# Kernel optimization log

Measured on AMD Instinct MI355X. Metric: run time of the kernel, lower is better.

## Reference

```python
import jax, jax.numpy as jnp
import numpy as np
import math

B, S, D, H, L, V, MAXLEN = 4, 2047, 256, 8, 2, 32000, 2048
DK = D // H
DFF = 2 * D
EPS = 1e-5


def make_pe(max_len, d):
    pos = jnp.arange(max_len, dtype=jnp.float32)[:, None]
    div = jnp.exp(jnp.arange(0, d, 2, dtype=jnp.float32) * (-math.log(10000.0) / d))
    pe = jnp.zeros((max_len, d), dtype=jnp.float32)
    pe = pe.at[:, 0::2].set(jnp.sin(pos * div))
    pe = pe.at[:, 1::2].set(jnp.cos(pos * div))
    return pe[None]  # [1, max_len, d]


def setup_inputs() -> dict:
    key = jax.random.key(0)
    ks = jax.random.split(key, 16)
    s = 0.02
    T = S + 1
    return {
        "embeddings": jax.random.normal(ks[0], (B, D), jnp.float32),
        "output_tokens": jax.random.randint(ks[1], (B, S), 0, V, jnp.int64),
        "causal_mask": jnp.tril(jnp.ones((T, T), jnp.int32))[None, None],  # [1,1,T,T]
        "key_padding_mask": jnp.ones((B, 1, 1, T), jnp.int32),
        "tok_emb": jax.random.normal(ks[2], (V, D), jnp.float32) * s,
        "pe": make_pe(MAXLEN, D),
        "Wq": jax.random.normal(ks[3], (L, D, D), jnp.float32) * s,
        "Wk": jax.random.normal(ks[4], (L, D, D), jnp.float32) * s,
        "Wv": jax.random.normal(ks[5], (L, D, D), jnp.float32) * s,
        "Wo": jax.random.normal(ks[6], (L, D, D), jnp.float32) * s,
        "bo": jnp.zeros((L, D), jnp.float32),
        "ln1_g": jnp.ones((L, D), jnp.float32),
        "ln1_b": jnp.zeros((L, D), jnp.float32),
        "W1": jax.random.normal(ks[7], (L, D, DFF), jnp.float32) * s,
        "b1": jnp.zeros((L, DFF), jnp.float32),
        "W2": jax.random.normal(ks[8], (L, DFF, D), jnp.float32) * s,
        "b2": jnp.zeros((L, D), jnp.float32),
        "ln2_g": jnp.ones((L, D), jnp.float32),
        "ln2_b": jnp.zeros((L, D), jnp.float32),
    }


def layer_norm(x, g, b):
    mu = jnp.mean(x, axis=-1, keepdims=True)
    var = jnp.mean(jnp.square(x - mu), axis=-1, keepdims=True)
    return (x - mu) * jax.lax.rsqrt(var + EPS) * g + b


def attention(x, Wq, Wk, Wv, Wo, bo, causal_mask, key_padding_mask):
    b, t, d = x.shape
    q = (x @ Wq).reshape(b, t, H, DK)
    k = (x @ Wk).reshape(b, t, H, DK)
    v = (x @ Wv).reshape(b, t, H, DK)
    scores = jnp.einsum('bqhd,bkhd->bhqk', q, k) / math.sqrt(DK)  # [B,H,T,T]
    neg = jnp.float32(-jnp.inf)
    scores = jnp.where(causal_mask == 0, neg, scores)
    scores = jnp.where(key_padding_mask == 0, neg, scores)
    attn = jax.nn.softmax(scores, axis=-1)
    out = jnp.einsum('bhqk,bkhd->bqhd', attn, v).reshape(b, t, d)
    return out @ Wo + bo


def reference(embeddings, output_tokens, causal_mask, key_padding_mask,
              tok_emb, pe, Wq, Wk, Wv, Wo, bo, ln1_g, ln1_b,
              W1, b1, W2, b2, ln2_g, ln2_b):
    emb_tok = tok_emb[output_tokens]                       # [B,S,D]
    x = jnp.concatenate([embeddings[:, None, :], emb_tok], axis=1)  # [B,T,D]
    x = x + pe[:, :x.shape[1]]
    for l in range(L):
        a = attention(x, Wq[l], Wk[l], Wv[l], Wo[l], bo[l], causal_mask, key_padding_mask)
        x = layer_norm(x + a, ln1_g[l], ln1_b[l])
        ff = jax.nn.relu(x @ W1[l] + b1[l]) @ W2[l] + b2[l]
        x = layer_norm(x + ff, ln2_g[l], ln2_b[l])
    return x[:, 1:, :]  # drop the prepended embedding position
```

## Files before the change

### kernel.cpp

```cpp
#include <hip/hip_runtime.h>
#include <cstdint>
#include <cstddef>

#define B_   4
#define S_   2047
#define T_   2048
#define D_   256
#define H_   8
#define DK_  32
#define DFF_ 512
#define L_   2

typedef short          s8v  __attribute__((ext_vector_type(8)));
typedef float          f4v  __attribute__((ext_vector_type(4)));
typedef unsigned short u8v  __attribute__((ext_vector_type(8)));
typedef unsigned int   u2v  __attribute__((ext_vector_type(2)));
typedef unsigned int   uint32;

union U8 { u8v v; unsigned short e[8]; };

__device__ __forceinline__ float bf2f(unsigned short h) {
    unsigned int u = ((unsigned int)h) << 16;
    float f; __builtin_memcpy(&f, &u, 4); return f;
}
__device__ __forceinline__ unsigned short f2bf(float f) {
    unsigned int u; __builtin_memcpy(&u, &f, 4);
    u += 0x7fffu + ((u >> 16) & 1u);
    return (unsigned short)(u >> 16);
}
__device__ __forceinline__ uint32 pack_bf2(float lo, float hi) {
    uint32 a, b;
    __builtin_memcpy(&a, &lo, 4); __builtin_memcpy(&b, &hi, 4);
    a += 0x8000u; b += 0x8000u;
    return __builtin_amdgcn_perm(b, a, 0x07060302);
}

#define QSCALE2 0.25503485951542068f

__global__ __launch_bounds__(256) void prep_k(
    const float* __restrict__ emb, const int* __restrict__ toks,
    const float* __restrict__ tokE, const float* __restrict__ pe,
    unsigned short* __restrict__ X,
    const float* __restrict__ Wq, const float* __restrict__ Wk,
    const float* __restrict__ Wv, const float* __restrict__ Wo,
    const float* __restrict__ W1, const float* __restrict__ W2,
    unsigned short* __restrict__ WqkvT, unsigned short* __restrict__ WoT,
    unsigned short* __restrict__ W1T, unsigned short* __restrict__ W2T)
{
    __shared__ float tile[32][33];
    if (blockIdx.x < 1024) {
        int idx = blockIdx.x * 256 + threadIdx.x;
        int d8 = (idx & 31) * 8;
        int t  = (idx >> 5) & (T_ - 1);
        int b  = idx >> 16;
        const float* src = (t == 0) ? (emb + b * D_)
                                    : (tokE + (size_t)toks[b * S_ + t - 1] * D_);
        const float* p = pe + (size_t)t * D_ + d8;
        U8 o;
#pragma unroll
        for (int j = 0; j < 8; ++j) o.e[j] = f2bf(src[d8 + j] + p[j]);
        *(u8v*)(X + (size_t)(b * T_ + t) * D_ + d8) = o.v;
        return;
    }
    int idx = blockIdx.x - 1024;
    const float* src; unsigned short* dst; int R, C, tr, tc;
    if (idx < 512) {
        int w = idx >> 7, rem = idx & 127, l = rem >> 6, t = rem & 63;
        tr = t >> 3; tc = t & 7; R = 256; C = 256;
        src = (w == 0 ? Wq : w == 1 ? Wk : w == 2 ? Wv : Wo) + (size_t)l * 65536;
        dst = (w < 3) ? WqkvT + (size_t)l * 196608 + (size_t)w * 65536
                      : WoT + (size_t)l * 65536;
    } else if (idx < 768) {
        int rem = idx - 512, l = rem >> 7, t = rem & 127;
        tr = t >> 4; tc = t & 15; R = 256; C = 512;
        src = W1 + (size_t)l * 131072; dst = W1T + (size_t)l * 131072;
    } else {
        int rem = idx - 768, l = rem >> 7, t = rem & 127;
        tr = t >> 3; tc = t & 7; R = 512; C = 256;
        src = W2 + (size_t)l * 131072; dst = W2T + (size_t)l * 131072;
    }
    int x = threadIdx.x & 31, y = threadIdx.x >> 5;
    int r0 = tr * 32, c0 = tc * 32;
#pragma unroll
    for (int i = 0; i < 32; i += 8) tile[y + i][x] = src[(size_t)(r0 + y + i) * C + c0 + x];
    __syncthreads();
#pragma unroll
    for (int i = 0; i < 32; i += 8)
        dst[(size_t)(c0 + y + i) * R + r0 + x] = f2bf(tile[x][y + i]);
}

__global__ __launch_bounds__(256) void gemm64_k(
    const unsigned short* __restrict__ A, const unsigned short* __restrict__ WT,
    const float* __restrict__ bias,
    unsigned short* __restrict__ oq, unsigned short* __restrict__ ok,
    unsigned short* __restrict__ ov, unsigned short* __restrict__ out,
    int K, int Ntot, int mode)
{
    __shared__ unsigned short At[64 * 72];
    __shared__ unsigned short Wt[64 * 72];
    const int tid = threadIdx.x;
    const int wave = tid >> 6, lane = tid & 63, l15 = lane & 15, quad = lane >> 4;
    const int m0 = blockIdx.x * 64, n0g = blockIdx.y * 64;

    f4v acc[4];
#pragma unroll
    for (int i = 0; i < 4; ++i) acc[i] = (f4v){0.f, 0.f, 0.f, 0.f};

    const int arow = tid >> 2, acg = (tid & 3) * 16;
    const unsigned short* ag = A + (size_t)(m0 + arow) * K + acg;
    const unsigned short* wg = WT + (size_t)(n0g + arow) * K + acg;
    u8v a0 = *(const u8v*)ag, a1 = *(const u8v*)(ag + 8);
    u8v w0 = *(const u8v*)wg, w1 = *(const u8v*)(wg + 8);

    const int niter = K >> 6;
    for (int kk = 0; kk < niter; ++kk) {
        *(u8v*)&At[arow * 72 + acg] = a0; *(u8v*)&At[arow * 72 + acg + 8] = a1;
        *(u8v*)&Wt[arow * 72 + acg] = w0; *(u8v*)&Wt[arow * 72 + acg + 8] = w1;
        __syncthreads();
        if (kk + 1 < niter) {
            int o = (kk + 1) * 64;
            a0 = *(const u8v*)(ag + o); a1 = *(const u8v*)(ag + o + 8);
            w0 = *(const u8v*)(wg + o); w1 = *(const u8v*)(wg + o + 8);
        }
#pragma unroll
        for (int ks = 0; ks < 2; ++ks) {
            s8v aF = *(const s8v*)&At[(wave * 16 + l15) * 72 + ks * 32 + quad * 8];
#pragma unroll
            for (int nt = 0; nt < 4; ++nt) {
                s8v wF = *(const s8v*)&Wt[(nt * 16 + l15) * 72 + ks * 32 + quad * 8];
                acc[nt] = __builtin_amdgcn_mfma_f32_16x16x32_bf16(aF, wF, acc[nt], 0, 0, 0);
            }
        }
        __syncthreads();
    }

    const int b = m0 >> 11, t0 = m0 & (T_ - 1);
    if (mode == 0) {
        int sub = blockIdx.y >> 2;
        int cb  = (blockIdx.y & 3) * 64;
        if (sub < 2) {
            unsigned short* dst = sub ? ok : oq;
            float sc = sub ? 1.f : QSCALE2;
#pragma unroll
            for (int nt = 0; nt < 4; ++nt) {
                int c = cb + nt * 16 + l15, hh = c >> 5, dk = c & 31;
#pragma unroll
                for (int r = 0; r < 4; ++r) {
                    int t = t0 + wave * 16 + quad * 4 + r;
                    dst[((size_t)(b * H_ + hh) * T_ + t) * DK_ + dk] = f2bf(acc[nt][r] * sc);
                }
            }
        } else {
            unsigned short* Vb = At;
#pragma unroll
            for (int nt = 0; nt < 4; ++nt) {
                int base = (nt * 16 + l15) * 72 + wave * 16 + quad * 4;
                *(uint32*)&Vb[base]     = pack_bf2(acc[nt][0], acc[nt][1]);
                *(uint32*)&Vb[base + 2] = pack_bf2(acc[nt][2], acc[nt][3]);
            }
            __syncthreads();
            int c = tid >> 2, chunk = tid & 3;
            int cg = cb + c, hh = cg >> 5, dk = cg & 31;
            unsigned short* dst = ov + ((size_t)(b * H_ + hh) * DK_ + dk) * T_ + t0 + chunk * 16;
            u8v v0 = *(u8v*)&Vb[c * 72 + chunk * 16];
            u8v v1 = *(u8v*)&Vb[c * 72 + chunk * 16 + 8];
            *(u8v*)dst = v0; *(u8v*)(dst + 8) = v1;
        }
    } else {
#pragma unroll
        for (int nt = 0; nt < 4; ++nt) {
            int c = n0g + nt * 16 + l15;
            float bv = bias[c];
#pragma unroll
            for (int r = 0; r < 4; ++r) {
                float v = acc[nt][r] + bv;
                v = v > 0.f ? v : 0.f;
                out[(size_t)(m0 + wave * 16 + quad * 4 + r) * Ntot + c] = f2bf(v);
            }
        }
    }
}

__global__ __launch_bounds__(1024, 4) void tail32_k(
    const unsigned short* __restrict__ AO,
    const unsigned short* __restrict__ WoTl, const float* __restrict__ bo,
    const unsigned short* __restrict__ Xres,
    const float* __restrict__ g1, const float* __restrict__ be1,
    const unsigned short* __restrict__ W1Tl, const float* __restrict__ b1,
    const unsigned short* __restrict__ W2Tl, const float* __restrict__ b2,
    const float* __restrict__ g2, const float* __restrict__ be2,
    unsigned short* __restrict__ Xout, float* __restrict__ fout, int last)
{
    __shared__ unsigned short Wt[256 * 72];
    __shared__ unsigned short As[32 * 72];
    __shared__ unsigned short X1s[32 * 264];
    __shared__ unsigned short Hs[32 * 520];
    __shared__ float LNsc[512];

    const int tid = threadIdx.x;
    const int wave = tid >> 6, lane = tid & 63, l15 = lane & 15, quad = lane >> 4;
    const int wr = wave >> 3, wc = wave & 7;
    const int m0 = blockIdx.x * 32;
    const int rbase = wr * 16 + quad * 4;

    const int wrow = tid >> 2, wcol = (tid & 3) * 16;
    const int arow = tid >> 3, acol = (tid & 7) * 8;

    f4v acc[2];
    u8v w0, w1, a0 = {0,0,0,0,0,0,0,0};

    const unsigned short* wgo = WoTl + (size_t)wrow * 256 + wcol;
    const unsigned short* wg1 = W1Tl + (size_t)wrow * 256 + wcol;
    const unsigned short* wg1b = W1Tl + (size_t)(256 + wrow) * 256 + wcol;
    const unsigned short* wg2 = W2Tl + (size_t)wrow * 512 + wcol;
    const unsigned short* ag  = AO + (size_t)(m0 + arow) * 256 + acol;

#define LDW(p, o) { w0 = *(const u8v*)((p)+(o)); w1 = *(const u8v*)((p)+(o)+8); }
#define STW { *(u8v*)&Wt[wrow*72+wcol] = w0; *(u8v*)&Wt[wrow*72+wcol+8] = w1; }

#pragma unroll
    for (int i = 0; i < 2; ++i) acc[i] = (f4v){0.f, 0.f, 0.f, 0.f};
    LDW(wgo, 0);
    if (tid < 256) a0 = *(const u8v*)ag;
    for (int kk = 0; kk < 4; ++kk) {
        STW;
        if (tid < 256) *(u8v*)&As[arow * 72 + acol] = a0;
        __syncthreads();
        if (kk < 3) {
            LDW(wgo, (kk + 1) * 64);
            if (tid < 256) a0 = *(const u8v*)(ag + (kk + 1) * 64);
        } else {
            LDW(wg1, 0);
        }
#pragma unroll
        for (int ks = 0; ks < 2; ++ks) {
            s8v aF = *(const s8v*)&As[(wr * 16 + l15) * 72 + ks * 32 + quad * 8];
#pragma unroll
            for (int nt = 0; nt < 2; ++nt) {
                s8v wF = *(const s8v*)&Wt[(wc * 32 + nt * 16 + l15) * 72 + ks * 32 + quad * 8];
                acc[nt] = __builtin_amdgcn_mfma_f32_16x16x32_bf16(aF, wF, acc[nt], 0, 0, 0);
            }
        }
        __syncthreads();
    }
    {
        float ps[4] = {0,0,0,0}, pq[4] = {0,0,0,0};
#pragma unroll
        for (int nt = 0; nt < 2; ++nt) {
            int c = wc * 32 + nt * 16 + l15;
            float bv = bo[c];
#pragma unroll
            for (int r = 0; r < 4; ++r) {
                float v = acc[nt][r] + bv + bf2f(Xres[(size_t)(m0 + rbase + r) * D_ + c]);
                acc[nt][r] = v; ps[r] += v; pq[r] += v * v;
            }
        }
#pragma unroll
        for (int r = 0; r < 4; ++r) {
            float s = ps[r], q = pq[r];
            s += __shfl_xor(s, 1); q += __shfl_xor(q, 1);
            s += __shfl_xor(s, 2); q += __shfl_xor(q, 2);
            s += __shfl_xor(s, 4); q += __shfl_xor(q, 4);
            s += __shfl_xor(s, 8); q += __shfl_xor(q, 8);
            if (l15 == 0) { LNsc[(rbase + r) * 8 + wc] = s; LNsc[256 + (rbase + r) * 8 + wc] = q; }
        }
        __syncthreads();
#pragma unroll
        for (int r = 0; r < 4; ++r) {
            int row = rbase + r;
            float s = 0.f, q = 0.f;
#pragma unroll
            for (int j = 0; j < 8; ++j) { s += LNsc[row * 8 + j]; q += LNsc[256 + row * 8 + j]; }
            float m = s * (1.f / 256.f);
            float rs = rsqrtf(q * (1.f / 256.f) - m * m + 1e-5f);
#pragma unroll
            for (int nt = 0; nt < 2; ++nt) {
                int c = wc * 32 + nt * 16 + l15;
                X1s[row * 264 + c] = f2bf((acc[nt][r] - m) * rs * g1[c] + be1[c]);
            }
        }
        __syncthreads();
    }

#pragma unroll
    for (int i = 0; i < 2; ++i) acc[i] = (f4v){0.f, 0.f, 0.f, 0.f};
    for (int kk = 0; kk < 4; ++kk) {
        STW;
        __syncthreads();
        if (kk < 3) LDW(wg1, (kk + 1) * 64) else LDW(wg1b, 0);
#pragma unroll
        for (int ks = 0; ks < 2; ++ks) {
            s8v aF = *(const s8v*)&X1s[(wr * 16 + l15) * 264 + kk * 64 + ks * 32 + quad * 8];
#pragma unroll
            for (int nt = 0; nt < 2; ++nt) {
                s8v wF = *(const s8v*)&Wt[(wc * 32 + nt * 16 + l15) * 72 + ks * 32 + quad * 8];
                acc[nt] = __builtin_amdgcn_mfma_f32_16x16x32_bf16(aF, wF, acc[nt], 0, 0, 0);
            }
        }
        __syncthreads();
    }
#pragma unroll
    for (int nt = 0; nt < 2; ++nt) {
        int c = wc * 32 + nt * 16 + l15;
        float bv = b1[c];
#pragma unroll
        for (int r = 0; r < 4; ++r) {
            float v = acc[nt][r] + bv; v = v > 0.f ? v : 0.f;
            Hs[(rbase + r) * 520 + c] = f2bf(v);
        }
    }

#pragma unroll
    for (int i = 0; i < 2; ++i) acc[i] = (f4v){0.f, 0.f, 0.f, 0.f};
    for (int kk = 0; kk < 4; ++kk) {
        STW;
        __syncthreads();
        if (kk < 3) LDW(wg1b, (kk + 1) * 64) else LDW(wg2, 0);
#pragma unroll
        for (int ks = 0; ks < 2; ++ks) {
            s8v aF = *(const s8v*)&X1s[(wr * 16 + l15) * 264 + kk * 64 + ks * 32 + quad * 8];
#pragma unroll
            for (int nt = 0; nt < 2; ++nt) {
                s8v wF = *(const s8v*)&Wt[(wc * 32 + nt * 16 + l15) * 72 + ks * 32 + quad * 8];
                acc[nt] = __builtin_amdgcn_mfma_f32_16x16x32_bf16(aF, wF, acc[nt], 0, 0, 0);
            }
        }
        __syncthreads();
    }
#pragma unroll
    for (int nt = 0; nt < 2; ++nt) {
        int c = wc * 32 + nt * 16 + l15;
        float bv = b1[256 + c];
#pragma unroll
        for (int r = 0; r < 4; ++r) {
            float v = acc[nt][r] + bv; v = v > 0.f ? v : 0.f;
            Hs[(rbase + r) * 520 + 256 + c] = f2bf(v);
        }
    }

#pragma unroll
    for (int i = 0; i < 2; ++i) acc[i] = (f4v){0.f, 0.f, 0.f, 0.f};
    for (int kk = 0; kk < 8; ++kk) {
        STW;
        __syncthreads();
        if (kk < 7) LDW(wg2, (kk + 1) * 64);
#pragma unroll
        for (int ks = 0; ks < 2; ++ks) {
            s8v aF = *(const s8v*)&Hs[(wr * 16 + l15) * 520 + kk * 64 + ks * 32 + quad * 8];
#pragma unroll
            for (int nt = 0; nt < 2; ++nt) {
                s8v wF = *(const s8v*)&Wt[(wc * 32 + nt * 16 + l15) * 72 + ks * 32 + quad * 8];
                acc[nt] = __builtin_amdgcn_mfma_f32_16x16x32_bf16(aF, wF, acc[nt], 0, 0, 0);
            }
        }
        __syncthreads();
    }
    {
        float ps[4] = {0,0,0,0}, pq[4] = {0,0,0,0};
#pragma unroll
        for (int nt = 0; nt < 2; ++nt) {
            int c = wc * 32 + nt * 16 + l15;
            float bv = b2[c];
#pragma unroll
            for (int r = 0; r < 4; ++r) {
                float v = acc[nt][r] + bv + bf2f(X1s[(rbase + r) * 264 + c]);
                acc[nt][r] = v; ps[r] += v; pq[r] += v * v;
            }
        }
#pragma unroll
        for (int r = 0; r < 4; ++r) {
            float s = ps[r], q = pq[r];
            s += __shfl_xor(s, 1); q += __shfl_xor(q, 1);
            s += __shfl_xor(s, 2); q += __shfl_xor(q, 2);
            s += __shfl_xor(s, 4); q += __shfl_xor(q, 4);
            s += __shfl_xor(s, 8); q += __shfl_xor(q, 8);
            if (l15 == 0) { LNsc[(rbase + r) * 8 + wc] = s; LNsc[256 + (rbase + r) * 8 + wc] = q; }
        }
        __syncthreads();
#pragma unroll
        for (int r = 0; r < 4; ++r) {
            int row = rbase + r;
            float s = 0.f, q = 0.f;
#pragma unroll
            for (int j = 0; j < 8; ++j) { s += LNsc[row * 8 + j]; q += LNsc[256 + row * 8 + j]; }
            float m = s * (1.f / 256.f);
            float rs = rsqrtf(q * (1.f / 256.f) - m * m + 1e-5f);
#pragma unroll
            for (int nt = 0; nt < 2; ++nt) {
                int c = wc * 32 + nt * 16 + l15;
                float val = (acc[nt][r] - m) * rs * g2[c] + be2[c];
                if (!last) {
                    Xout[(size_t)(m0 + row) * D_ + c] = f2bf(val);
                } else {
                    int gr = m0 + row;
                    int t = gr & (T_ - 1), bb = gr >> 11;
                    if (t) fout[((size_t)bb * S_ + t - 1) * D_ + c] = val;
                }
            }
        }
    }
#undef LDW
#undef STW
}

#define KTP 5120
#define VTP 4864
__global__ __launch_bounds__(512, 4) void attn_k(
    const unsigned short* __restrict__ Qh, const unsigned short* __restrict__ Kh,
    const unsigned short* __restrict__ VT, unsigned short* __restrict__ AO)
{
    __shared__ unsigned short Kt[2 * KTP];
    __shared__ unsigned short Vt[2 * VTP];
    __shared__ unsigned short Ps[8][16 * 136];

    const int tid = threadIdx.x, wave = tid >> 6, lane = tid & 63;
    const int l15 = lane & 15, quad = lane >> 4;
    const int grp = wave >> 2, wl = wave & 3;

    const int bid = blockIdx.x;
    const int bh = bid >> 4;
    const int x  = (bid < 256) ? (bid & 15) : 15 - (bid & 15);
    const int b = bh >> 3, h = bh & 7;
    const size_t hoff = (size_t)bh * T_ * DK_;
    unsigned short* Pw = &Ps[wave][0];

    const int qt = grp ? 31 - x : x;
    const int nkt = qt / 2 + 1;
    const int nmax = (31 - x) / 2 + 1;

    const int krow = tid >> 2, kcol = (tid & 3) * 8;
    const int vdk = tid >> 4, vc = (tid & 15) * 8;
    const unsigned short* kgp = Kh + hoff + (size_t)krow * DK_ + kcol;
    const unsigned short* vgp = VT + ((size_t)bh * DK_ + vdk) * T_ + vc;

    u8v kr = *(const u8v*)kgp;
    u8v vr = *(const u8v*)vgp;

    const int q0w = qt * 64 + wl * 16;
    const s8v qB = *(const s8v*)(Qh + hoff + (size_t)(q0w + l15) * DK_ + quad * 8);
    f4v O0 = {0,0,0,0}, O1 = {0,0,0,0};
    f4v Lacc = {0,0,0,0};
    const short one_bf = (short)0x3F80;
    const s8v vOne = { one_bf, one_bf, one_bf, one_bf,
                       one_bf, one_bf, one_bf, one_bf };

    for (int kt = 0; kt < nmax; ++kt) {
        unsigned short* Ktb = Kt + (kt & 1) * KTP;
        unsigned short* Vtb = Vt + (kt & 1) * VTP;
        *(u8v*)&Ktb[krow * 40 + kcol] = kr;
        *(u8v*)&Vtb[vdk * 152 + vc]   = vr;
        __syncthreads();
        if (kt + 1 < nmax) {
            kr = *(const u8v*)(kgp + (size_t)(kt + 1) * 128 * DK_);
            vr = *(const u8v*)(vgp + (kt + 1) * 128);
        }
        if (kt < nkt) {
            const int k0 = kt * 128;
            f4v s[8];
            f4v zero = {0,0,0,0};
#pragma unroll
            for (int nt = 0; nt < 8; ++nt) {
                s8v kA = *(const s8v*)&Ktb[(nt * 16 + l15) * 40 + quad * 8];
                s[nt] = __builtin_amdgcn_mfma_f32_16x16x32_bf16(kA, qB, zero, 0, 0, 0);
            }
            if (kt == nkt - 1) {
                int query = q0w + l15;
#pragma unroll
                for (int nt = 0; nt < 8; ++nt)
#pragma unroll
                    for (int r = 0; r < 4; ++r) {
                        int key = k0 + nt * 16 + quad * 4 + r;
                        if (key > query) s[nt][r] = -1e30f;
                    }
            }
#pragma unroll
            for (int nt = 0; nt < 8; ++nt)
#pragma unroll
                for (int r = 0; r < 4; ++r)
                    s[nt][r] = exp2f(s[nt][r]);
#pragma unroll
            for (int nt = 0; nt < 8; ++nt) {
                u2v pw;
                pw.x = pack_bf2(s[nt][0], s[nt][1]);
                pw.y = pack_bf2(s[nt][2], s[nt][3]);
                *(u2v*)&Pw[l15 * 136 + nt * 16 + quad * 4] = pw;
            }
#pragma unroll
            for (int ks = 0; ks < 4; ++ks) {
                s8v aP = *(const s8v*)&Pw[l15 * 136 + ks * 32 + quad * 8];
                s8v v0 = *(const s8v*)&Vtb[l15 * 152 + ks * 32 + quad * 8];
                s8v v1 = *(const s8v*)&Vtb[(16 + l15) * 152 + ks * 32 + quad * 8];
                O0 = __builtin_amdgcn_mfma_f32_16x16x32_bf16(aP, v0, O0, 0, 0, 0);
                O1 = __builtin_amdgcn_mfma_f32_16x16x32_bf16(aP, v1, O1, 0, 0, 0);
                Lacc = __builtin_amdgcn_mfma_f32_16x16x32_bf16(aP, vOne, Lacc, 0, 0, 0);
            }
            if (kt == nkt - 1) {
#pragma unroll
                for (int r = 0; r < 4; ++r) {
                    float linv = 1.f / Lacc[r];
                    int row = q0w + quad * 4 + r;
                    size_t base = (size_t)(b * T_ + row) * D_ + h * DK_;
                    AO[base + l15]      = f2bf(O0[r] * linv);
                    AO[base + 16 + l15] = f2bf(O1[r] * linv);
                }
            }
        }
    }
}

extern "C" void kernel_launch(void* const* d_in, const int* in_sizes, int n_in,
                              void* d_out, int out_size, void* d_ws, size_t ws_size,
                              hipStream_t stream)
{
    const float* emb  = (const float*)d_in[0];
    const int*   toks = (const int*)d_in[1];
    const float* tokE = (const float*)d_in[4];
    const float* pe   = (const float*)d_in[5];
    const float* Wq   = (const float*)d_in[6];
    const float* Wk   = (const float*)d_in[7];
    const float* Wv   = (const float*)d_in[8];
    const float* Wo   = (const float*)d_in[9];
    const float* bo   = (const float*)d_in[10];
    const float* g1   = (const float*)d_in[11];
    const float* be1  = (const float*)d_in[12];
    const float* W1   = (const float*)d_in[13];
    const float* b1   = (const float*)d_in[14];
    const float* W2   = (const float*)d_in[15];
    const float* b2   = (const float*)d_in[16];
    const float* g2   = (const float*)d_in[17];
    const float* be2  = (const float*)d_in[18];
    float* out = (float*)d_out;

    unsigned short* ws = (unsigned short*)d_ws;
    size_t off = 0;
    const size_t XSZ = (size_t)B_ * T_ * D_;
    unsigned short* Xa    = ws + off; off += XSZ;
    unsigned short* Xb    = ws + off; off += XSZ;
    unsigned short* Qh    = ws + off; off += XSZ;
    unsigned short* Kh    = ws + off; off += XSZ;
    unsigned short* VTb   = ws + off; off += XSZ;
    unsigned short* AOb   = ws + off; off += XSZ;
    unsigned short* Hb    = ws + off; off += (size_t)B_ * T_ * DFF_;
    unsigned short* WqkvT = ws + off; off += (size_t)L_ * 3 * D_ * D_;
    unsigned short* WoT   = ws + off; off += (size_t)L_ * D_ * D_;
    unsigned short* W1T   = ws + off; off += (size_t)L_ * D_ * DFF_;
    unsigned short* W2T   = ws + off; off += (size_t)L_ * DFF_ * D_;
    (void)ws_size; (void)in_sizes; (void)n_in; (void)out_size;
    (void)Xb; (void)Hb;

    prep_k<<<dim3(2048), 256, 0, stream>>>(emb, toks, tokE, pe, Xa,
                                           Wq, Wk, Wv, Wo, W1, W2,
                                           WqkvT, WoT, W1T, W2T);

    for (int l = 0; l < L_; ++l) {
        const unsigned short* wqkv = WqkvT + (size_t)l * 3 * D_ * D_;
        const unsigned short* wo   = WoT + (size_t)l * D_ * D_;
        const unsigned short* w1   = W1T + (size_t)l * D_ * DFF_;
        const unsigned short* w2   = W2T + (size_t)l * DFF_ * D_;
        const int last = (l == L_ - 1);

        gemm64_k<<<dim3(128, 12), 256, 0, stream>>>(Xa, wqkv, nullptr,
                                                    Qh, Kh, VTb, nullptr, D_, D_, 0);
        attn_k<<<dim3(512), 512, 0, stream>>>(Qh, Kh, VTb, AOb);
        tail32_k<<<dim3(256), 1024, 0, stream>>>(AOb, wo, bo + l * D_, Xa,
                                                 g1 + l * D_, be1 + l * D_,
                                                 w1, b1 + l * DFF_,
                                                 w2, b2 + l * D_,
                                                 g2 + l * D_, be2 + l * D_,
                                                 Xa, out, last);
    }
}
```

Before: 242.2 us.

## Load attention K/V fragments straight from global memory, dropping LDS staging

The attention kernel no longer stages K and V tiles into double-buffered shared memory behind a block-wide barrier. Each wave now reads its MFMA operand fragments for K and the transposed V directly from global memory and loops only over its own causal tile count, so the two wave groups no longer march in lockstep. Launch bounds are raised to allow more resident blocks per CU, since LDS use is much lower. The cost is redundant global and L2 traffic, because all eight waves reload the same K/V data, and the loads are less coalesced, latency-exposed 16-byte reads with no prefetch.

```diff
diff --git a/kernel.cpp b/kernel.cpp
--- a/kernel.cpp
+++ b/kernel.cpp
@@ -403,14 +403,10 @@
 #undef STW
 }
 
-#define KTP 5120
-#define VTP 4864
-__global__ __launch_bounds__(512, 4) void attn_k(
+__global__ __launch_bounds__(512, 8) void attn_k(
     const unsigned short* __restrict__ Qh, const unsigned short* __restrict__ Kh,
     const unsigned short* __restrict__ VT, unsigned short* __restrict__ AO)
 {
-    __shared__ unsigned short Kt[2 * KTP];
-    __shared__ unsigned short Vt[2 * VTP];
     __shared__ unsigned short Ps[8][16 * 136];
 
     const int tid = threadIdx.x, wave = tid >> 6, lane = tid & 63;
@@ -426,15 +422,9 @@
 
     const int qt = grp ? 31 - x : x;
     const int nkt = qt / 2 + 1;
-    const int nmax = (31 - x) / 2 + 1;
-
-    const int krow = tid >> 2, kcol = (tid & 3) * 8;
-    const int vdk = tid >> 4, vc = (tid & 15) * 8;
-    const unsigned short* kgp = Kh + hoff + (size_t)krow * DK_ + kcol;
-    const unsigned short* vgp = VT + ((size_t)bh * DK_ + vdk) * T_ + vc;
-
-    u8v kr = *(const u8v*)kgp;
-    u8v vr = *(const u8v*)vgp;
+
+    const unsigned short* kfp = Kh + hoff + (size_t)l15 * DK_ + quad * 8;
+    const unsigned short* vfp = VT + ((size_t)bh * DK_ + l15) * T_ + quad * 8;
 
     const int q0w = qt * 64 + wl * 16;
     const s8v qB = *(const s8v*)(Qh + hoff + (size_t)(q0w + l15) * DK_ + quad * 8);
@@ -444,67 +434,54 @@
     const s8v vOne = { one_bf, one_bf, one_bf, one_bf,
                        one_bf, one_bf, one_bf, one_bf };
 
-    for (int kt = 0; kt < nmax; ++kt) {
-        unsigned short* Ktb = Kt + (kt & 1) * KTP;
-        unsigned short* Vtb = Vt + (kt & 1) * VTP;
-        *(u8v*)&Ktb[krow * 40 + kcol] = kr;
-        *(u8v*)&Vtb[vdk * 152 + vc]   = vr;
-        __syncthreads();
-        if (kt + 1 < nmax) {
-            kr = *(const u8v*)(kgp + (size_t)(kt + 1) * 128 * DK_);
-            vr = *(const u8v*)(vgp + (kt + 1) * 128);
-        }
-        if (kt < nkt) {
-            const int k0 = kt * 128;
-            f4v s[8];
-            f4v zero = {0,0,0,0};
-#pragma unroll
-            for (int nt = 0; nt < 8; ++nt) {
-                s8v kA = *(const s8v*)&Ktb[(nt * 16 + l15) * 40 + quad * 8];
-                s[nt] = __builtin_amdgcn_mfma_f32_16x16x32_bf16(kA, qB, zero, 0, 0, 0);
-            }
-            if (kt == nkt - 1) {
-                int query = q0w + l15;
-#pragma unroll
-                for (int nt = 0; nt < 8; ++nt)
-#pragma unroll
-                    for (int r = 0; r < 4; ++r) {
-                        int key = k0 + nt * 16 + quad * 4 + r;
-                        if (key > query) s[nt][r] = -1e30f;
-                    }
-            }
+    for (int kt = 0; kt < nkt; ++kt) {
+        const int k0 = kt * 128;
+        f4v s[8];
+        f4v zero = {0,0,0,0};
+#pragma unroll
+        for (int nt = 0; nt < 8; ++nt) {
+            s8v kA = *(const s8v*)(kfp + (size_t)(k0 + nt * 16) * DK_);
+            s[nt] = __builtin_amdgcn_mfma_f32_16x16x32_bf16(kA, qB, zero, 0, 0, 0);
+        }
+        if (kt == nkt - 1) {
+            int query = q0w + l15;
 #pragma unroll
             for (int nt = 0; nt < 8; ++nt)
 #pragma unroll
-                for (int r = 0; r < 4; ++r)
-                    s[nt][r] = exp2f(s[nt][r]);
-#pragma unroll
-            for (int nt = 0; nt < 8; ++nt) {
-                u2v pw;
-                pw.x = pack_bf2(s[nt][0], s[nt][1]);
-                pw.y = pack_bf2(s[nt][2], s[nt][3]);
-                *(u2v*)&Pw[l15 * 136 + nt * 16 + quad * 4] = pw;
-            }
-#pragma unroll
-            for (int ks = 0; ks < 4; ++ks) {
-                s8v aP = *(const s8v*)&Pw[l15 * 136 + ks * 32 + quad * 8];
-                s8v v0 = *(const s8v*)&Vtb[l15 * 152 + ks * 32 + quad * 8];
-                s8v v1 = *(const s8v*)&Vtb[(16 + l15) * 152 + ks * 32 + quad * 8];
-                O0 = __builtin_amdgcn_mfma_f32_16x16x32_bf16(aP, v0, O0, 0, 0, 0);
-                O1 = __builtin_amdgcn_mfma_f32_16x16x32_bf16(aP, v1, O1, 0, 0, 0);
-                Lacc = __builtin_amdgcn_mfma_f32_16x16x32_bf16(aP, vOne, Lacc, 0, 0, 0);
-            }
-            if (kt == nkt - 1) {
-#pragma unroll
                 for (int r = 0; r < 4; ++r) {
-                    float linv = 1.f / Lacc[r];
-                    int row = q0w + quad * 4 + r;
-                    size_t base = (size_t)(b * T_ + row) * D_ + h * DK_;
-                    AO[base + l15]      = f2bf(O0[r] * linv);
-                    AO[base + 16 + l15] = f2bf(O1[r] * linv);
+                    int key = k0 + nt * 16 + quad * 4 + r;
+                    if (key > query) s[nt][r] = -1e30f;
                 }
-            }
-        }
+        }
+#pragma unroll
+        for (int nt = 0; nt < 8; ++nt)
+#pragma unroll
+            for (int r = 0; r < 4; ++r)
+                s[nt][r] = exp2f(s[nt][r]);
+#pragma unroll
+        for (int nt = 0; nt < 8; ++nt) {
+            u2v pw;
+            pw.x = pack_bf2(s[nt][0], s[nt][1]);
+            pw.y = pack_bf2(s[nt][2], s[nt][3]);
+            *(u2v*)&Pw[l15 * 136 + nt * 16 + quad * 4] = pw;
+        }
+#pragma unroll
+        for (int ks = 0; ks < 4; ++ks) {
+            s8v aP = *(const s8v*)&Pw[l15 * 136 + ks * 32 + quad * 8];
+            s8v v0 = *(const s8v*)(vfp + k0 + ks * 32);
+            s8v v1 = *(const s8v*)(vfp + (size_t)16 * T_ + k0 + ks * 32);
+            O0 = __builtin_amdgcn_mfma_f32_16x16x32_bf16(aP, v0, O0, 0, 0, 0);
+            O1 = __builtin_amdgcn_mfma_f32_16x16x32_bf16(aP, v1, O1, 0, 0, 0);
+            Lacc = __builtin_amdgcn_mfma_f32_16x16x32_bf16(aP, vOne, Lacc, 0, 0, 0);
+        }
+    }
+#pragma unroll
+    for (int r = 0; r < 4; ++r) {
+        float linv = 1.f / Lacc[r];
+        int row = q0w + quad * 4 + r;
+        size_t base = (size_t)(b * T_ + row) * D_ + h * DK_;
+        AO[base + l15]      = f2bf(O0[r] * linv);
+        AO[base + 16 + l15] = f2bf(O1[r] * linv);
     }
 }
 
```

New measurement: 336.9 us. +39.1%, slower.
